# Performance work log

Measured on AMD Instinct MI355X. Metric: run time of the kernel, lower is better.

The kernel has to match this reference:

```python
import jax, jax.numpy as jnp
import numpy as np


def setup_inputs() -> dict:
    key = jax.random.key(0)
    B, L, F = 32, 128, 64
    x = jax.random.normal(key, (B, L, F), dtype=jnp.float32)
    return {"x": x}


def reference(x):
    # Original: einsum('...if,ikl->...klf', x, M) where M[i,k,l] is one-hot:
    #   for k in [0, L):   M[i, k, (i+k)%L] = 1  -> out[..., k, l, :] = x[..., (l-k)%L, :]
    #   for k in [L, 2L):  M[i, k, (k-i)%L] = 1  -> out[..., k, l, :] = x[..., (k-l)%L, :]
    # i.e. a cyclic shift for the first L slices and a reflected shift for the next L.
    L = x.shape[-2]
    k_shift = jnp.arange(L)[:, None]            # (L, 1)
    l = jnp.arange(L)[None, :]                  # (1, L)
    idx_shift = (l - k_shift) % L               # (L, L) cyclic shifts
    k_refl = jnp.arange(L, 2 * L)[:, None]      # (L, 1)
    idx_refl = (k_refl - l) % L                 # (L, L) reflected shifts
    idx = jnp.concatenate([idx_shift, idx_refl], axis=0)  # (2L, L)
    # gather along the L axis: (..., L, F) -> (..., 2L, L, F)
    return jnp.take(x, idx, axis=-2)
```

## Files before the change

### kernel.cpp

```cpp
#include <hip/hip_runtime.h>


__global__ __launch_bounds__(256) void SymmetryExpansion_kernel(
    const float4* __restrict__ x, float4* __restrict__ out) {
    unsigned tid  = threadIdx.x;
    unsigned f4   = tid & 15u;
    unsigned i_lo = tid >> 4;

    unsigned blk  = blockIdx.x;
    unsigned i_hi = blk & 7u;
    unsigned kc   = (blk >> 3) & 7u;
    unsigned b    = blk >> 6;

    unsigned i     = (i_hi << 4) | i_lo;
    unsigned kbase = kc << 5;

    unsigned l0 = ((kbase < 128u) ? (i + kbase) : (kbase - i)) & 127u;

    float4 v = x[(b << 11) | (i << 4) | f4];

    unsigned base = (b << 19) | (kbase << 11) | f4;
#pragma unroll
    for (unsigned kk = 0; kk < 32u; ++kk) {
        unsigned l = (l0 + kk) & 127u;
        out[base + (kk << 11) + (l << 4)] = v;
    }
}

extern "C" void kernel_launch(void* const* d_in, const int* in_sizes, int n_in,
                              void* d_out, int out_size, void* d_ws, size_t ws_size,
                              hipStream_t stream) {
    const float4* x = (const float4*)d_in[0];
    float4* out = (float4*)d_out;
    dim3 grid(2048), block(256);
    hipLaunchKernelGGL(SymmetryExpansion_kernel, grid, block, 0, stream, x, out);
}
```

Before: 251.3 us.

## Reorganize gather so each block writes contiguous output rows with register reuse

```diff
diff --git a/kernel.cpp b/kernel.cpp
--- a/kernel.cpp
+++ b/kernel.cpp
@@ -3,27 +3,38 @@
 
 __global__ __launch_bounds__(256) void SymmetryExpansion_kernel(
     const float4* __restrict__ x, float4* __restrict__ out) {
-    unsigned tid  = threadIdx.x;
-    unsigned f4   = tid & 15u;
-    unsigned i_lo = tid >> 4;
+    unsigned t  = threadIdx.x;
+    unsigned f4 = t & 15u;
+    unsigned w  = t >> 4;
 
-    unsigned blk  = blockIdx.x;
-    unsigned i_hi = blk & 7u;
-    unsigned kc   = (blk >> 3) & 7u;
-    unsigned b    = blk >> 6;
+    unsigned blk   = blockIdx.x;
+    unsigned kbsel = blk & 31u;
+    unsigned b     = blk >> 5;
 
-    unsigned i     = (i_hi << 4) | i_lo;
-    unsigned kbase = kc << 5;
+    bool refl   = (kbsel >= 16u);
+    unsigned kb = refl ? (kbsel + 112u) : kbsel;
 
-    unsigned l0 = ((kbase < 128u) ? (i + kbase) : (kbase - i)) & 127u;
+    unsigned rbase = refl ? (kb - w) : (w + 128u - kb);
 
-    float4 v = x[(b << 11) | (i << 4) | f4];
+    const float4* xb = x + (b << 11) + f4;
+    float4 r[8];
+#pragma unroll
+    for (unsigned j = 0; j < 8u; ++j)
+        r[j] = xb[((rbase + (j << 4)) & 127u) << 4];
 
-    unsigned base = (b << 19) | (kbase << 11) | f4;
+    float4* ob = out + (b << 19) + (kb << 11) + t;
+    if (!refl) {
 #pragma unroll
-    for (unsigned kk = 0; kk < 32u; ++kk) {
-        unsigned l = (l0 + kk) & 127u;
-        out[base + (kk << 11) + (l << 4)] = v;
+        for (unsigned m = 0; m < 8u; ++m)
+#pragma unroll
+            for (unsigned j2 = 0; j2 < 8u; ++j2)
+                ob[(m << 15) + (j2 << 8)] = r[(j2 - m) & 7u];
+    } else {
+#pragma unroll
+        for (unsigned m = 0; m < 8u; ++m)
+#pragma unroll
+            for (unsigned j2 = 0; j2 < 8u; ++j2)
+                ob[(m << 15) + (j2 << 8)] = r[(m - j2) & 7u];
     }
 }
 
@@ -32,6 +43,6 @@
                               hipStream_t stream) {
     const float4* x = (const float4*)d_in[0];
     float4* out = (float4*)d_out;
-    dim3 grid(2048), block(256);
+    dim3 grid(1024), block(256);
     hipLaunchKernelGGL(SymmetryExpansion_kernel, grid, block, 0, stream, x, out);
 }
```

New measurement: 255.7 us. About the same (+1.8%).
